# Performance work log

Hardware: AMD Instinct MI355X
Metric: run time of the kernel (lower is better)

## Reference

```python
import jax, jax.numpy as jnp
import numpy as np

ALPHA = 0.5      # sklearn Lasso(alpha=0.5)
N_ITERS = 50     # fixed FISTA iterations
N_POWER = 10     # power iterations for Lipschitz estimate


def _soft(x, thr):
    return jnp.sign(x) * jnp.maximum(jnp.abs(x) - thr, 0.0)


def setup_inputs() -> dict:
    key = jax.random.key(0)
    k1, k2 = jax.random.split(key)
    B, n_rx, n_tx, n_carrier = 8, 4, 32, 256
    M = 256
    D = n_rx * n_tx * n_carrier * 2  # 65536
    x = jax.random.normal(k1, (B, n_rx, n_tx, n_carrier, 2), jnp.float32)
    coding_mat = jax.random.normal(k2, (B, M, D), jnp.float32)
    return {"x": x, "coding_mat": coding_mat}


def _lasso_fista(x, coding_mat):
    B = x.shape[0]
    M = coding_mat.shape[1]
    D = coding_mat.shape[2]
    shape = x.shape
    w_true = x.reshape(B, D)                       # (nrx ntx channel complex) flatten
    y = jnp.einsum('bmd,bd->bm', coding_mat, w_true)  # compressed measurements

    # Lipschitz constant of grad of (1/(2M))||y - Aw||^2 via power iteration on A^T A / M
    def power_step(_, v):
        Av = jnp.einsum('bmd,bd->bm', coding_mat, v)
        v = jnp.einsum('bmd,bm->bd', coding_mat, Av)
        return v / (jnp.linalg.norm(v, axis=-1, keepdims=True) + 1e-12)

    v = jnp.full((B, D), 1.0 / np.sqrt(D), dtype=x.dtype)
    v = jax.lax.fori_loop(0, N_POWER, power_step, v)
    Av = jnp.einsum('bmd,bd->bm', coding_mat, v)
    L = jnp.einsum('bm,bm->b', Av, Av) / M        # rayleigh quotient, v unit norm
    L = jax.lax.stop_gradient(L)[:, None]          # [B,1] step-size constant

    w0 = jnp.zeros((B, D), x.dtype)

    def fista_step(carry, _):
        w, z, t = carry
        r = jnp.einsum('bmd,bd->bm', coding_mat, z) - y
        grad = jnp.einsum('bmd,bm->bd', coding_mat, r) / M
        w_new = _soft(z - grad / L, ALPHA / L)
        t_new = 0.5 * (1.0 + jnp.sqrt(1.0 + 4.0 * t * t))
        z_new = w_new + ((t - 1.0) / t_new) * (w_new - w)
        return (w_new, z_new, t_new), None

    (w, _, _), _ = jax.lax.scan(fista_step, (w0, w0, jnp.float32(1.0)), None, length=N_ITERS)
    return w.reshape(shape)


def reference(x, coding_mat):
    return _lasso_fista(x, coding_mat)
```

## Files before the change

### kernel.cpp

```cpp
#include <hip/hip_runtime.h>
#include <hip/hip_fp16.h>
#include <math.h>

#define B 8
#define M 256
#define D 65536

static constexpr float ALPHA = 0.5f;
static constexpr int N_ITERS = 50;
static constexpr int N_POWER = 10;

__global__ __launch_bounds__(256) void k_conv(const float* __restrict__ A,
                                              __half* __restrict__ Ah) {
    const size_t n8 = (size_t)B * M * D / 8;
    size_t stride = (size_t)gridDim.x * 256;
    for (size_t i = (size_t)blockIdx.x * 256 + threadIdx.x; i < n8; i += stride) {
        float4 f0 = ((const float4*)A)[2 * i];
        float4 f1 = ((const float4*)A)[2 * i + 1];
        union { uint4 u; __half2 h[4]; } o;
        o.h[0] = __floats2half2_rn(f0.x, f0.y);
        o.h[1] = __floats2half2_rn(f0.z, f0.w);
        o.h[2] = __floats2half2_rn(f1.x, f1.y);
        o.h[3] = __floats2half2_rn(f1.z, f1.w);
        ((uint4*)Ah)[i] = o.u;
    }
}

__global__ __launch_bounds__(256) void k_y_u0(const __half* __restrict__ Ah,
                                              const float* __restrict__ x,
                                              float* __restrict__ y,
                                              float* __restrict__ u) {
    int bm = blockIdx.x;
    int b = bm >> 8;
    const uint4* arow = (const uint4*)(Ah + (size_t)bm * D);
    const float4* xrow = (const float4*)(x + (size_t)b * D);
    float sy = 0.f, ss = 0.f;
#pragma unroll 4
    for (int i = threadIdx.x; i < D / 8; i += 256) {
        uint4 a = arow[i];
        const __half2* hp = (const __half2*)&a;
        float4 x0 = xrow[2 * i], x1 = xrow[2 * i + 1];
        float2 f0 = __half22float2(hp[0]);
        float2 f1 = __half22float2(hp[1]);
        float2 f2 = __half22float2(hp[2]);
        float2 f3 = __half22float2(hp[3]);
        sy += f0.x * x0.x + f0.y * x0.y + f1.x * x0.z + f1.y * x0.w +
              f2.x * x1.x + f2.y * x1.y + f3.x * x1.z + f3.y * x1.w;
        ss += f0.x + f0.y + f1.x + f1.y + f2.x + f2.y + f3.x + f3.y;
    }
    __shared__ float sdata[8];
    for (int off = 32; off > 0; off >>= 1) {
        sy += __shfl_down(sy, off, 64);
        ss += __shfl_down(ss, off, 64);
    }
    int lane = threadIdx.x & 63, wid = threadIdx.x >> 6;
    if (lane == 0) { sdata[wid] = sy; sdata[4 + wid] = ss; }
    __syncthreads();
    if (threadIdx.x == 0) {
        y[bm] = sdata[0] + sdata[1] + sdata[2] + sdata[3];
        u[bm] = (sdata[4] + sdata[5] + sdata[6] + sdata[7]) * 0.00390625f;
    }
}

__global__ __launch_bounds__(256) void k_gram(const __half* __restrict__ Ah,
                                              float* __restrict__ G) {
    const int PI[10] = {0, 0, 0, 0, 1, 1, 1, 2, 2, 3};
    const int PJ[10] = {0, 1, 2, 3, 1, 2, 3, 2, 3, 3};
    int idx = blockIdx.x;
    int ch = idx & 15; idx >>= 4;
    int p = idx % 10;
    int b = idx / 10;
    int ti = PI[p] * 64, tj = PJ[p] * 64;
    int k0 = ch * 4096;

    __shared__ __align__(16) float As[16][68];
    __shared__ __align__(16) float Bs[16][68];

    int t = threadIdx.x;
    int lrow = t >> 2;
    int lk = (t & 3) << 2;
    int r0 = (t >> 4) << 2;
    int c0 = (t & 15) << 2;

    const __half* Ab = Ah + (size_t)b * M * D;
    float acc[4][4] = {};

    for (int ks = 0; ks < 4096; ks += 16) {
        uint2 au = *(const uint2*)(Ab + (size_t)(ti + lrow) * D + k0 + ks + lk);
        uint2 bu = *(const uint2*)(Ab + (size_t)(tj + lrow) * D + k0 + ks + lk);
        const __half2* ah = (const __half2*)&au;
        const __half2* bh = (const __half2*)&bu;
        float2 a0 = __half22float2(ah[0]), a1 = __half22float2(ah[1]);
        float2 b0 = __half22float2(bh[0]), b1 = __half22float2(bh[1]);
        __syncthreads();
        As[lk + 0][lrow] = a0.x; As[lk + 1][lrow] = a0.y;
        As[lk + 2][lrow] = a1.x; As[lk + 3][lrow] = a1.y;
        Bs[lk + 0][lrow] = b0.x; Bs[lk + 1][lrow] = b0.y;
        Bs[lk + 2][lrow] = b1.x; Bs[lk + 3][lrow] = b1.y;
        __syncthreads();
#pragma unroll
        for (int k = 0; k < 16; ++k) {
            float4 a = *(const float4*)&As[k][r0];
            float4 c = *(const float4*)&Bs[k][c0];
            float avv[4] = {a.x, a.y, a.z, a.w};
            float cvv[4] = {c.x, c.y, c.z, c.w};
#pragma unroll
            for (int i = 0; i < 4; ++i)
#pragma unroll
                for (int j = 0; j < 4; ++j)
                    acc[i][j] += avv[i] * cvv[j];
        }
    }
    float* Gb = G + (size_t)b * M * M;
    bool offdiag = (ti != tj);
#pragma unroll
    for (int i = 0; i < 4; ++i)
#pragma unroll
        for (int j = 0; j < 4; ++j) {
            atomicAdd(&Gb[(size_t)(ti + r0 + i) * M + (tj + c0 + j)], acc[i][j]);
            if (offdiag)
                atomicAdd(&Gb[(size_t)(tj + c0 + j) * M + (ti + r0 + i)], acc[i][j]);
        }
}

__global__ __launch_bounds__(256) void k_power(const float* __restrict__ G,
                                               const float* __restrict__ u0,
                                               float* __restrict__ Lp) {
    int b = blockIdx.x;
    int m = threadIdx.x;
    __shared__ float su[M];
    __shared__ float red[4];
    su[m] = u0[b * M + m];
    __syncthreads();
    const float* Gb = G + (size_t)b * M * M;
    for (int it = 0; it < N_POWER; ++it) {
        float gm = 0.f;
        const float4* grow = (const float4*)(Gb + (size_t)m * M);
#pragma unroll 8
        for (int k = 0; k < M / 4; ++k) {
            float4 g = grow[k];
            gm += g.x * su[4 * k] + g.y * su[4 * k + 1] + g.z * su[4 * k + 2] +
                  g.w * su[4 * k + 3];
        }
        float part = su[m] * gm;
        for (int off = 32; off > 0; off >>= 1) part += __shfl_down(part, off, 64);
        if ((m & 63) == 0) red[m >> 6] = part;
        __syncthreads();
        float n = sqrtf(red[0] + red[1] + red[2] + red[3]);
        float inv = 1.f / (n + 1e-12f);
        su[m] = gm * inv;
        __syncthreads();
    }
    float part = su[m] * su[m];
    for (int off = 32; off > 0; off >>= 1) part += __shfl_down(part, off, 64);
    if ((m & 63) == 0) red[m >> 6] = part;
    __syncthreads();
    if (m == 0) {
        float L = (red[0] + red[1] + red[2] + red[3]) * (1.0f / 256.0f);
        Lp[b * 4 + 0] = L;
        Lp[b * 4 + 1] = 1.0f / (256.0f * L);
        Lp[b * 4 + 2] = ALPHA / L;
    }
}

__global__ __launch_bounds__(256) void k_cstep(const float* __restrict__ spart,
                                               const float* __restrict__ y,
                                               const float* __restrict__ Lp,
                                               float* __restrict__ c) {
    int blk = blockIdx.x;
    int b = blk >> 3;
    int mg = blk & 7;
    int t = threadIdx.x;
    int tm = t & 31;
    int cg = t >> 5;
    int m = mg * 32 + tm;
    const float* sp = spart + (size_t)b * 512 * M + m;
    float s = 0.f;
#pragma unroll 8
    for (int ch = cg; ch < 512; ch += 8)
        s += sp[(size_t)ch * M];
    __shared__ float red[8][32];
    red[cg][tm] = s;
    __syncthreads();
    if (t < 32) {
        float sv = red[0][t] + red[1][t] + red[2][t] + red[3][t] +
                   red[4][t] + red[5][t] + red[6][t] + red[7][t];
        int bm = b * M + mg * 32 + t;
        c[bm] = (sv - y[bm]) * Lp[b * 4 + 1];
    }
}

__global__ __launch_bounds__(256) void k_fista(const __half* __restrict__ Ah,
                                               const float* __restrict__ cc,
                                               const float* __restrict__ Lp,
                                               float* __restrict__ z,
                                               float* __restrict__ w,
                                               float* __restrict__ spart,
                                               float beta) {
    int cid = blockIdx.x;
    int b = cid >> 9;
    int chunk = cid & 511;
    int d0 = chunk << 7;
    int t = threadIdx.x;
    int dj = t & 15;
    int mi = t >> 4;

    __shared__ float sc[M];
    __shared__ float gws[4][16][8];
    __shared__ float znS[128];
    __shared__ float sred[M];

    sc[t] = cc[b * M + t];
    __syncthreads();

    const __half* Ap = Ah + (size_t)b * M * D + (size_t)mi * D + d0 + dj * 8;
    uint4 areg[16];
    float g[8] = {};
#pragma unroll
    for (int s = 0; s < 16; ++s) {
        areg[s] = *(const uint4*)(Ap + (size_t)(s * 16) * D);
        float cm = sc[s * 16 + mi];
        const __half2* hp = (const __half2*)&areg[s];
        float2 f0 = __half22float2(hp[0]);
        float2 f1 = __half22float2(hp[1]);
        float2 f2 = __half22float2(hp[2]);
        float2 f3 = __half22float2(hp[3]);
        g[0] = fmaf(f0.x, cm, g[0]); g[1] = fmaf(f0.y, cm, g[1]);
        g[2] = fmaf(f1.x, cm, g[2]); g[3] = fmaf(f1.y, cm, g[3]);
        g[4] = fmaf(f2.x, cm, g[4]); g[5] = fmaf(f2.y, cm, g[5]);
        g[6] = fmaf(f3.x, cm, g[6]); g[7] = fmaf(f3.y, cm, g[7]);
    }
#pragma unroll
    for (int j = 0; j < 8; ++j) {
        g[j] += __shfl_xor(g[j], 16, 64);
        g[j] += __shfl_xor(g[j], 32, 64);
    }
    int wv = t >> 6;
    if ((t & 63) < 16) {
#pragma unroll
        for (int j = 0; j < 8; ++j) gws[wv][dj][j] = g[j];
    }
    __syncthreads();

    if (t < 128) {
        int ldj = t >> 3, lj = t & 7;
        float gs = gws[0][ldj][lj] + gws[1][ldj][lj] +
                   gws[2][ldj][lj] + gws[3][ldj][lj];
        size_t zi = (size_t)b * D + d0 + t;
        float thr = Lp[b * 4 + 2];
        float zv = z[zi], wold = w[zi];
        float cand = zv - gs;
        float a1 = fabsf(cand) - thr;
        float wn = a1 > 0.f ? copysignf(a1, cand) : 0.f;
        float znv = wn + beta * (wn - wold);
        w[zi] = wn;
        z[zi] = znv;
        znS[t] = znv;
    }
    __syncthreads();

    float zr[8];
    {
        float4 z0 = *(const float4*)&znS[dj * 8];
        float4 z1 = *(const float4*)&znS[dj * 8 + 4];
        zr[0] = z0.x; zr[1] = z0.y; zr[2] = z0.z; zr[3] = z0.w;
        zr[4] = z1.x; zr[5] = z1.y; zr[6] = z1.z; zr[7] = z1.w;
    }
#pragma unroll
    for (int s = 0; s < 16; ++s) {
        const __half2* hp = (const __half2*)&areg[s];
        float2 f0 = __half22float2(hp[0]);
        float2 f1 = __half22float2(hp[1]);
        float2 f2 = __half22float2(hp[2]);
        float2 f3 = __half22float2(hp[3]);
        float p = f0.x * zr[0] + f0.y * zr[1] + f1.x * zr[2] + f1.y * zr[3] +
                  f2.x * zr[4] + f2.y * zr[5] + f3.x * zr[6] + f3.y * zr[7];
        p += __shfl_xor(p, 1, 64);
        p += __shfl_xor(p, 2, 64);
        p += __shfl_xor(p, 4, 64);
        p += __shfl_xor(p, 8, 64);
        if (dj == 0) sred[s * 16 + mi] = p;
    }
    __syncthreads();
    spart[((size_t)b * 512 + chunk) * M + t] = sred[t];
}

extern "C" void kernel_launch(void* const* d_in, const int* in_sizes, int n_in,
                              void* d_out, int out_size, void* d_ws, size_t ws_size,
                              hipStream_t stream) {
    (void)in_sizes; (void)n_in; (void)out_size; (void)ws_size;
    const float* x = (const float*)d_in[0];
    const float* A = (const float*)d_in[1];
    float* w = (float*)d_out;

    __half* Ah = (__half*)d_ws;
    float* ws = (float*)((char*)d_ws + (size_t)B * M * D * sizeof(__half));
    float* y  = ws;
    float* u  = ws + 2048;
    float* Lp = ws + 4096;
    float* c  = ws + 4128;
    float* z  = ws + 8192;
    float* G  = ws + 8192 + 524288;
    float* spart = G;

    hipMemsetAsync(G, 0, (size_t)B * M * M * sizeof(float), stream);
    hipMemsetAsync(z, 0, (size_t)B * D * sizeof(float), stream);
    hipMemsetAsync(w, 0, (size_t)B * D * sizeof(float), stream);

    k_conv<<<16384, 256, 0, stream>>>(A, Ah);
    k_y_u0<<<B * M, 256, 0, stream>>>(Ah, x, y, u);
    k_gram<<<B * 10 * 16, 256, 0, stream>>>(Ah, G);
    k_power<<<B, 256, 0, stream>>>(G, u, Lp);

    hipMemsetAsync(spart, 0, (size_t)B * 512 * M * sizeof(float), stream);

    double t = 1.0;
    for (int k = 0; k < N_ITERS; ++k) {
        double tn = 0.5 * (1.0 + sqrt(1.0 + 4.0 * t * t));
        float beta = (float)((t - 1.0) / tn);
        k_cstep<<<64, 256, 0, stream>>>(spart, y, Lp, c);
        k_fista<<<B * 512, 256, 0, stream>>>(Ah, c, Lp, z, w, spart, beta);
        t = tn;
    }
}
```

Baseline: 4.153 ms.

## Compute Gram matrix with MFMA fp16 and direct global-to-LDS loads

Replaces the scalar FP32 outer-product Gram kernel with a matrix-core version using 16x16x32 f16 MFMA instructions. It uses 128x128 tiles (3 upper-triangle pairs) with a 2048-wide K split, and loads tiles via global_load_lds straight into shared memory. This targets the compute-bound A·Aᵀ build used for the power iteration. The trade-offs are no double buffering and possible LDS bank conflicts from the unpadded layout, while the atomic accumulation into G is kept.

Measured after the change: 3.734 ms. 10.1% less time.

```diff
diff --git a/kernel.cpp b/kernel.cpp
--- a/kernel.cpp
+++ b/kernel.cpp
@@ -9,6 +9,9 @@
 static constexpr float ALPHA = 0.5f;
 static constexpr int N_ITERS = 50;
 static constexpr int N_POWER = 10;
+
+typedef _Float16 f16x8 __attribute__((ext_vector_type(8)));
+typedef float f32x4 __attribute__((ext_vector_type(4)));
 
 __global__ __launch_bounds__(256) void k_conv(const float* __restrict__ A,
                                               __half* __restrict__ Ah) {
@@ -62,65 +65,92 @@
     }
 }
 
-__global__ __launch_bounds__(256) void k_gram(const __half* __restrict__ Ah,
-                                              float* __restrict__ G) {
-    const int PI[10] = {0, 0, 0, 0, 1, 1, 1, 2, 2, 3};
-    const int PJ[10] = {0, 1, 2, 3, 1, 2, 3, 2, 3, 3};
-    int idx = blockIdx.x;
-    int ch = idx & 15; idx >>= 4;
-    int p = idx % 10;
-    int b = idx / 10;
-    int ti = PI[p] * 64, tj = PJ[p] * 64;
-    int k0 = ch * 4096;
-
-    __shared__ __align__(16) float As[16][68];
-    __shared__ __align__(16) float Bs[16][68];
+__global__ __launch_bounds__(256) void k_gram_mfma(const __half* __restrict__ Ah,
+                                                   float* __restrict__ G) {
+    int bx = blockIdx.x;
+    int ch = bx & 31;
+    int p  = (bx >> 5) % 3;
+    int b  = bx / 96;
+    const int PI[3] = {0, 0, 128};
+    const int PJ[3] = {0, 128, 128};
+    int ti = PI[p], tj = PJ[p];
+    int k0 = ch * 2048;
+
+    __shared__ __half As[128 * 32];
+    __shared__ __half Bs[128 * 32];
 
     int t = threadIdx.x;
-    int lrow = t >> 2;
-    int lk = (t & 3) << 2;
-    int r0 = (t >> 4) << 2;
-    int c0 = (t & 15) << 2;
+    int w = t >> 6, lane = t & 63;
+    int wr = w >> 1, wc = w & 1;
 
     const __half* Ab = Ah + (size_t)b * M * D;
-    float acc[4][4] = {};
-
-    for (int ks = 0; ks < 4096; ks += 16) {
-        uint2 au = *(const uint2*)(Ab + (size_t)(ti + lrow) * D + k0 + ks + lk);
-        uint2 bu = *(const uint2*)(Ab + (size_t)(tj + lrow) * D + k0 + ks + lk);
-        const __half2* ah = (const __half2*)&au;
-        const __half2* bh = (const __half2*)&bu;
-        float2 a0 = __half22float2(ah[0]), a1 = __half22float2(ah[1]);
-        float2 b0 = __half22float2(bh[0]), b1 = __half22float2(bh[1]);
+
+    int srow = w * 32 + (lane >> 2);
+    int scol = (lane & 3) * 8;
+
+    f32x4 acc[4][4];
+#pragma unroll
+    for (int i = 0; i < 4; ++i)
+#pragma unroll
+        for (int j = 0; j < 4; ++j)
+            acc[i][j] = (f32x4){0.f, 0.f, 0.f, 0.f};
+
+    int frow = lane & 15;
+    int koff = (lane >> 4) * 8;
+
+    for (int ks = 0; ks < 2048; ks += 32) {
         __syncthreads();
-        As[lk + 0][lrow] = a0.x; As[lk + 1][lrow] = a0.y;
-        As[lk + 2][lrow] = a1.x; As[lk + 3][lrow] = a1.y;
-        Bs[lk + 0][lrow] = b0.x; Bs[lk + 1][lrow] = b0.y;
-        Bs[lk + 2][lrow] = b1.x; Bs[lk + 3][lrow] = b1.y;
+        {
+            const __half* ga0 = Ab + (size_t)(ti + srow) * D + k0 + ks + scol;
+            const __half* ga1 = ga0 + (size_t)16 * D;
+            const __half* gb0 = Ab + (size_t)(tj + srow) * D + k0 + ks + scol;
+            const __half* gb1 = gb0 + (size_t)16 * D;
+            __builtin_amdgcn_global_load_lds(
+                (const __attribute__((address_space(1))) void*)ga0,
+                (__attribute__((address_space(3))) void*)&As[(w * 32) * 32], 16, 0, 0);
+            __builtin_amdgcn_global_load_lds(
+                (const __attribute__((address_space(1))) void*)ga1,
+                (__attribute__((address_space(3))) void*)&As[(w * 32 + 16) * 32], 16, 0, 0);
+            __builtin_amdgcn_global_load_lds(
+                (const __attribute__((address_space(1))) void*)gb0,
+                (__attribute__((address_space(3))) void*)&Bs[(w * 32) * 32], 16, 0, 0);
+            __builtin_amdgcn_global_load_lds(
+                (const __attribute__((address_space(1))) void*)gb1,
+                (__attribute__((address_space(3))) void*)&Bs[(w * 32 + 16) * 32], 16, 0, 0);
+        }
         __syncthreads();
-#pragma unroll
-        for (int k = 0; k < 16; ++k) {
-            float4 a = *(const float4*)&As[k][r0];
-            float4 c = *(const float4*)&Bs[k][c0];
-            float avv[4] = {a.x, a.y, a.z, a.w};
-            float cvv[4] = {c.x, c.y, c.z, c.w};
-#pragma unroll
-            for (int i = 0; i < 4; ++i)
-#pragma unroll
-                for (int j = 0; j < 4; ++j)
-                    acc[i][j] += avv[i] * cvv[j];
-        }
-    }
+
+        f16x8 aF[4], bF[4];
+#pragma unroll
+        for (int i = 0; i < 4; ++i)
+            aF[i] = *(const f16x8*)&As[(wr * 64 + i * 16 + frow) * 32 + koff];
+#pragma unroll
+        for (int j = 0; j < 4; ++j)
+            bF[j] = *(const f16x8*)&Bs[(wc * 64 + j * 16 + frow) * 32 + koff];
+#pragma unroll
+        for (int i = 0; i < 4; ++i)
+#pragma unroll
+            for (int j = 0; j < 4; ++j)
+                acc[i][j] = __builtin_amdgcn_mfma_f32_16x16x32_f16(
+                    aF[i], bF[j], acc[i][j], 0, 0, 0);
+    }
+
     float* Gb = G + (size_t)b * M * M;
-    bool offdiag = (ti != tj);
+    bool offd = (ti != tj);
+    int r0 = (lane >> 4) * 4;
+    int c0 = lane & 15;
 #pragma unroll
     for (int i = 0; i < 4; ++i)
 #pragma unroll
-        for (int j = 0; j < 4; ++j) {
-            atomicAdd(&Gb[(size_t)(ti + r0 + i) * M + (tj + c0 + j)], acc[i][j]);
-            if (offdiag)
-                atomicAdd(&Gb[(size_t)(tj + c0 + j) * M + (ti + r0 + i)], acc[i][j]);
-        }
+        for (int j = 0; j < 4; ++j)
+#pragma unroll
+            for (int r = 0; r < 4; ++r) {
+                int gi = ti + wr * 64 + i * 16 + r0 + r;
+                int gj = tj + wc * 64 + j * 16 + c0;
+                float v = acc[i][j][r];
+                atomicAdd(&Gb[(size_t)gi * M + gj], v);
+                if (offd) atomicAdd(&Gb[(size_t)gj * M + gi], v);
+            }
 }
 
 __global__ __launch_bounds__(256) void k_power(const float* __restrict__ G,
@@ -309,7 +339,7 @@
 
     k_conv<<<16384, 256, 0, stream>>>(A, Ah);
     k_y_u0<<<B * M, 256, 0, stream>>>(Ah, x, y, u);
-    k_gram<<<B * 10 * 16, 256, 0, stream>>>(Ah, G);
+    k_gram_mfma<<<8 * 3 * 32, 256, 0, stream>>>(Ah, G);
     k_power<<<B, 256, 0, stream>>>(G, u, Lp);
 
     hipMemsetAsync(spart, 0, (size_t)B * 512 * M * sizeof(float), stream);
```
